# Kernel optimization log

Hardware: AMD Instinct MI355X
Metric: run time of the kernel (lower is better)

Reference implementation:

```python
import jax, jax.numpy as jnp
import numpy as np

P, A = 100000, 50000          # num papers, num authors
IN, H, OUT = 128, 256, 349    # in_channels, hidden_channels, out_channels
E_W, E_C = 600000, 1000000    # writes edges, cites edges


def setup_inputs() -> dict:
    key = jax.random.key(0)
    ks = jax.random.split(key, 24)
    s = 0.05  # weight init scale
    inp = {
        "x_paper": jax.random.normal(ks[0], (P, IN), jnp.float32),
        "emb_author": jax.random.normal(ks[1], (A, H), jnp.float32) * s,
        "lin_paper_w": jax.random.normal(ks[2], (IN, H), jnp.float32) * s,
        "lin_paper_b": jnp.zeros((H,), jnp.float32),
        "c0_root_paper_w": jax.random.normal(ks[3], (H, H), jnp.float32) * s,
        "c0_root_paper_b": jnp.zeros((H,), jnp.float32),
        "c0_root_author_w": jax.random.normal(ks[4], (H, H), jnp.float32) * s,
        "c0_root_author_b": jnp.zeros((H,), jnp.float32),
        "c0_rel_writes_w": jax.random.normal(ks[5], (H, H), jnp.float32) * s,
        "c0_rel_cites_w": jax.random.normal(ks[6], (H, H), jnp.float32) * s,
        "c0_rel_revw_w": jax.random.normal(ks[7], (H, H), jnp.float32) * s,
        "c1_root_w": jax.random.normal(ks[8], (H, OUT), jnp.float32) * s,
        "c1_root_b": jnp.zeros((OUT,), jnp.float32),
        "c1_rel_writes_w": jax.random.normal(ks[9], (H, OUT), jnp.float32) * s,
        "c1_rel_cites_w": jax.random.normal(ks[10], (H, OUT), jnp.float32) * s,
        "writes_src": jax.random.randint(ks[11], (E_W,), 0, A, jnp.int32),
        "writes_dst": jax.random.randint(ks[12], (E_W,), 0, P, jnp.int32),
        "cites_src": jax.random.randint(ks[13], (E_C,), 0, P, jnp.int32),
        "cites_dst": jax.random.randint(ks[14], (E_C,), 0, P, jnp.int32),
        "revw_src": jax.random.randint(ks[15], (E_W,), 0, P, jnp.int32),
        "revw_dst": jax.random.randint(ks[16], (E_W,), 0, A, jnp.int32),
    }
    return inp


def mean_agg(x_src, src, dst, num_dst):
    """adj_t.matmul(x, reduce='mean'): mean of source features over in-edges per dst node (0 for isolated nodes)."""
    msg = jnp.take(x_src, src, axis=0)                                  # [E, D]
    summed = jax.ops.segment_sum(msg, dst, num_segments=num_dst)        # [num_dst, D]
    cnt = jax.ops.segment_sum(jnp.ones((dst.shape[0],), x_src.dtype), dst, num_segments=num_dst)
    return summed / jnp.maximum(cnt, 1.0)[:, None]


def reference(x_paper, emb_author, lin_paper_w, lin_paper_b,
              c0_root_paper_w, c0_root_paper_b, c0_root_author_w, c0_root_author_b,
              c0_rel_writes_w, c0_rel_cites_w, c0_rel_revw_w,
              c1_root_w, c1_root_b, c1_rel_writes_w, c1_rel_cites_w,
              writes_src, writes_dst, cites_src, cites_dst, revw_src, revw_dst):
    # input projection for featured type; embedding for author
    h_p = x_paper @ lin_paper_w + lin_paper_b   # [P, H]
    h_a = emb_author                            # [A, H]

    # layer 0: root transforms + per-relation mean-agg + rel linear, accumulated by dst type
    out_p = h_p @ c0_root_paper_w + c0_root_paper_b
    out_a = h_a @ c0_root_author_w + c0_root_author_b
    out_p = out_p + mean_agg(h_a, writes_src, writes_dst, P) @ c0_rel_writes_w
    out_p = out_p + mean_agg(h_p, cites_src, cites_dst, P) @ c0_rel_cites_w
    out_a = out_a + mean_agg(h_p, revw_src, revw_dst, A) @ c0_rel_revw_w
    h_p = jax.nn.relu(out_p)
    h_a = jax.nn.relu(out_a)
    # dropout is a no-op in eval mode

    # final layer: only out_type='paper' and edge types ending at paper
    out = h_p @ c1_root_w + c1_root_b
    out = out + mean_agg(h_a, writes_src, writes_dst, P) @ c1_rel_writes_w
    out = out + mean_agg(h_p, cites_src, cites_dst, P) @ c1_rel_cites_w
    return jax.nn.log_softmax(out, axis=-1)
```

## Files before the change

kernel.cpp:

```cpp
#include <hip/hip_runtime.h>
#include <cstdint>
#include <cstddef>

#define P_NODES 100000
#define A_NODES 50000
#define IN_CH   128
#define H_CH    256
#define OUT_CH  349
#define NE_W    600000
#define NE_C    1000000

#define SCAN_BS 512

typedef unsigned short u16;
typedef unsigned int   u32;
typedef __bf16 bf16x8 __attribute__((ext_vector_type(8)));
typedef float  f32x4  __attribute__((ext_vector_type(4)));
typedef u16    u16x4  __attribute__((ext_vector_type(4)));
typedef u16    u16x8  __attribute__((ext_vector_type(8)));

__device__ __forceinline__ u16 f2bf(float f) {
    u32 u = __builtin_bit_cast(u32, f);
    u += 0x7FFFu + ((u >> 16) & 1u);
    return (u16)(u >> 16);
}
__device__ __forceinline__ float bf2f(u16 v) {
    return __builtin_bit_cast(float, (u32)v << 16);
}

typedef const __attribute__((address_space(1))) u32 gas_u32;
typedef __attribute__((address_space(3))) u32 las_u32;
__device__ __forceinline__ void gl_lds16(const void* g, void* l)
{
    __builtin_amdgcn_global_load_lds(
        reinterpret_cast<gas_u32*>(reinterpret_cast<uintptr_t>(g)),
        reinterpret_cast<las_u32*>(reinterpret_cast<uintptr_t>(l)),
        16, 0, 0);
}

template<bool OUTBF, bool RELU>
__global__ __launch_bounds__(256) void mfma_gemm(
    const u16* __restrict__ A, int lda,
    const u16* __restrict__ WT, int ldw,
    const float* __restrict__ bias, void* __restrict__ Cv, int ldc,
    int M, int N, int K)
{
    __shared__ u16 Asl[128 * 32];
    __shared__ u16 Bsl[128 * 32];

    const int tid = threadIdx.x;
    const int blockM = blockIdx.y * 128;
    const int blockN = blockIdx.x * 128;
    const int w    = tid >> 6;
    const int lane = tid & 63;
    const int m16  = lane & 15;
    const int quad = lane >> 4;
    const int wr   = (w >> 1) * 64;
    const int wc   = (w & 1) * 64;

    if (blockM + 128 > M || blockN + 128 > N) {
        for (int i = tid; i < 128 * 32; i += 256) { Asl[i] = 0; Bsl[i] = 0; }
    }
    __syncthreads();

    const int ra  = lane >> 2;
    const int rA0 = w * 32 + ra;
    const int rA1 = rA0 + 16;
    const int cs  = ((lane & 3) ^ ((rA0 >> 1) & 3)) * 8;

    const u16* gA0 = A  + (size_t)(blockM + rA0) * lda + cs;
    const u16* gA1 = A  + (size_t)(blockM + rA1) * lda + cs;
    const u16* gB0 = WT + (size_t)(blockN + rA0) * ldw + cs;
    const u16* gB1 = WT + (size_t)(blockN + rA1) * ldw + cs;
    u16* lA0 = &Asl[(w * 32) * 32];
    u16* lA1 = &Asl[(w * 32 + 16) * 32];
    u16* lB0 = &Bsl[(w * 32) * 32];
    u16* lB1 = &Bsl[(w * 32 + 16) * 32];
    const bool vA0 = blockM + rA0 < M, vA1 = blockM + rA1 < M;
    const bool vB0 = blockN + rA0 < N, vB1 = blockN + rA1 < N;

    const int swz = (quad ^ ((m16 >> 1) & 3)) * 8;

    f32x4 acc[4][4];
#pragma unroll
    for (int i = 0; i < 4; ++i)
#pragma unroll
        for (int j = 0; j < 4; ++j) acc[i][j] = (f32x4){0.f, 0.f, 0.f, 0.f};

    for (int k0 = 0; k0 < K; k0 += 32) {
        if (vA0) gl_lds16(gA0 + k0, lA0);
        if (vA1) gl_lds16(gA1 + k0, lA1);
        if (vB0) gl_lds16(gB0 + k0, lB0);
        if (vB1) gl_lds16(gB1 + k0, lB1);
        __syncthreads();

        bf16x8 af[4], bfr[4];
#pragma unroll
        for (int mt = 0; mt < 4; ++mt)
            af[mt] = *(const bf16x8*)&Asl[(wr + mt * 16 + m16) * 32 + swz];
#pragma unroll
        for (int nt = 0; nt < 4; ++nt)
            bfr[nt] = *(const bf16x8*)&Bsl[(wc + nt * 16 + m16) * 32 + swz];
#pragma unroll
        for (int mt = 0; mt < 4; ++mt)
#pragma unroll
            for (int nt = 0; nt < 4; ++nt)
                acc[mt][nt] = __builtin_amdgcn_mfma_f32_16x16x32_bf16(
                    af[mt], bfr[nt], acc[mt][nt], 0, 0, 0);
        __syncthreads();
    }

#pragma unroll
    for (int mt = 0; mt < 4; ++mt) {
#pragma unroll
        for (int nt = 0; nt < 4; ++nt) {
            int col = blockN + wc + nt * 16 + m16;
            if (col >= N) continue;
#pragma unroll
            for (int reg = 0; reg < 4; ++reg) {
                int row = blockM + wr + mt * 16 + quad * 4 + reg;
                if (row >= M) continue;
                float v = acc[mt][nt][reg];
                if (bias) v += bias[col];
                if constexpr (RELU) v = fmaxf(v, 0.f);
                size_t off = (size_t)row * ldc + col;
                if constexpr (OUTBF) ((u16*)Cv)[off] = f2bf(v);
                else                 ((float*)Cv)[off] = v;
            }
        }
    }
}

__global__ void prep_convert(const float* __restrict__ x, u16* __restrict__ x_bf,
                             const float* __restrict__ emb, u16* __restrict__ emb_bf)
{
    int i = blockIdx.x * blockDim.x + threadIdx.x;
    const int NX = P_NODES * IN_CH / 4;
    const int NE = A_NODES * H_CH / 4;
    if (i < NX) {
        float4 v = *(const float4*)(x + (size_t)i * 4);
        u16x4 o = {f2bf(v.x), f2bf(v.y), f2bf(v.z), f2bf(v.w)};
        *(u16x4*)(x_bf + (size_t)i * 4) = o;
    } else if (i < NX + NE) {
        int j = i - NX;
        int r = j >> 6, c = (j & 63) * 4;
        float4 v = *(const float4*)(emb + (size_t)r * H_CH + c);
        u16x4 o = {f2bf(v.x), f2bf(v.y), f2bf(v.z), f2bf(v.w)};
        *(u16x4*)(emb_bf + (size_t)r * 512 + c) = o;
    }
}

__global__ void transpose_all(
    const float* __restrict__ lin, const float* __restrict__ r0p,
    const float* __restrict__ c0wr, const float* __restrict__ c0ci,
    const float* __restrict__ r0a, const float* __restrict__ c0rv,
    const float* __restrict__ r1, const float* __restrict__ c1wr,
    const float* __restrict__ c1ci,
    u16* __restrict__ wt_lin, u16* __restrict__ wt_l0p,
    u16* __restrict__ wt_l0a, u16* __restrict__ wt_l1)
{
    int i = blockIdx.x * blockDim.x + threadIdx.x;
    const float* W; u16* WT; int N, ldk, koff;
    if (i < 32768)       { W = lin;  WT = wt_lin; N = 256; ldk = 128; koff = 0;   }
    else if (i < 98304)  { i -= 32768;  W = r0p;  WT = wt_l0p; N = 256; ldk = 768; koff = 0;   }
    else if (i < 163840) { i -= 98304;  W = c0wr; WT = wt_l0p; N = 256; ldk = 768; koff = 256; }
    else if (i < 229376) { i -= 163840; W = c0ci; WT = wt_l0p; N = 256; ldk = 768; koff = 512; }
    else if (i < 294912) { i -= 229376; W = r0a;  WT = wt_l0a; N = 256; ldk = 512; koff = 0;   }
    else if (i < 360448) { i -= 294912; W = c0rv; WT = wt_l0a; N = 256; ldk = 512; koff = 256; }
    else if (i < 449792) { i -= 360448; W = r1;   WT = wt_l1;  N = 349; ldk = 768; koff = 0;   }
    else if (i < 539136) { i -= 449792; W = c1wr; WT = wt_l1;  N = 349; ldk = 768; koff = 256; }
    else if (i < 628480) { i -= 539136; W = c1ci; WT = wt_l1;  N = 349; ldk = 768; koff = 512; }
    else return;
    int k = i / N, n = i - k * N;
    WT[(size_t)n * ldk + koff + k] = f2bf(W[(size_t)k * N + n]);
}

__global__ void deg3_kernel(const int* __restrict__ wd, const int* __restrict__ cd,
                            const int* __restrict__ rd,
                            int* __restrict__ deg_w, int* __restrict__ deg_c,
                            int* __restrict__ deg_r)
{
    int e = blockIdx.x * blockDim.x + threadIdx.x;
    if (e < NE_W) atomicAdd(&deg_w[wd[e]], 1);
    if (e < NE_C) atomicAdd(&deg_c[cd[e]], 1);
    if (e < NE_W) atomicAdd(&deg_r[rd[e]], 1);
}

__global__ __launch_bounds__(SCAN_BS) void scan_a3(
    const int* __restrict__ dw, const int* __restrict__ dc, const int* __restrict__ dr,
    int* __restrict__ pw, int* __restrict__ pc, int* __restrict__ pr, int* __restrict__ blk)
{
    __shared__ int s[SCAN_BS];
    int g = blockIdx.y;
    const int* deg = (g == 0) ? dw : (g == 1) ? dc : dr;
    int* ptr = (g == 0) ? pw : (g == 1) ? pc : pr;
    int n = (g == 2) ? A_NODES : P_NODES;
    int tid = threadIdx.x;
    int i = blockIdx.x * SCAN_BS + tid;
    int v = (i < n) ? deg[i] : 0;
    s[tid] = v;
    __syncthreads();
    for (int off = 1; off < SCAN_BS; off <<= 1) {
        int t = 0;
        if (tid >= off) t = s[tid - off];
        __syncthreads();
        s[tid] += t;
        __syncthreads();
    }
    if (i < n) ptr[i] = s[tid] - v;
    if (tid == SCAN_BS - 1) blk[g * 256 + blockIdx.x] = s[tid];
}

__global__ __launch_bounds__(SCAN_BS) void scan_b3(int* __restrict__ blk)
{
    __shared__ int s[SCAN_BS];
    int g = blockIdx.x;
    int tid = threadIdx.x;
    int v = (tid < 256) ? blk[g * 256 + tid] : 0;
    s[tid] = v;
    __syncthreads();
    for (int off = 1; off < SCAN_BS; off <<= 1) {
        int t = 0;
        if (tid >= off) t = s[tid - off];
        __syncthreads();
        s[tid] += t;
        __syncthreads();
    }
    if (tid < 256) blk[g * 256 + tid] = s[tid] - v;
}

__global__ void scan_c3(const int* __restrict__ dw, const int* __restrict__ dc,
                        const int* __restrict__ dr,
                        int* __restrict__ pw, int* __restrict__ pc, int* __restrict__ pr,
                        const int* __restrict__ blk,
                        int* __restrict__ cw, int* __restrict__ cc, int* __restrict__ cr,
                        float* __restrict__ iw, float* __restrict__ ic, float* __restrict__ ir)
{
    int g = blockIdx.y;
    const int* deg = (g == 0) ? dw : (g == 1) ? dc : dr;
    int* ptr = (g == 0) ? pw : (g == 1) ? pc : pr;
    int* cur = (g == 0) ? cw : (g == 1) ? cc : cr;
    float* inv = (g == 0) ? iw : (g == 1) ? ic : ir;
    int n = (g == 2) ? A_NODES : P_NODES;
    int E = (g == 1) ? NE_C : NE_W;
    int i = blockIdx.x * blockDim.x + threadIdx.x;
    if (i < n) {
        int p = ptr[i] + blk[g * 256 + i / SCAN_BS];
        ptr[i] = p;
        cur[i] = p;
        inv[i] = 1.0f / fmaxf((float)deg[i], 1.0f);
    }
    if (i == 0) ptr[n] = E;
}

__global__ __launch_bounds__(256) void fill3_kernel(
    const int* __restrict__ wsrc, const int* __restrict__ wdst,
    const int* __restrict__ csrc, const int* __restrict__ cdst,
    const int* __restrict__ rsrc, const int* __restrict__ rdst,
    int* __restrict__ cw, int* __restrict__ cc, int* __restrict__ cr,
    int* __restrict__ iw, int* __restrict__ ic, int* __restrict__ ir)
{
    const int g   = blockIdx.x & 7;
    const int bi  = blockIdx.x >> 3;
    const int nbt = (gridDim.x >> 3) * blockDim.x;
    const int t0  = bi * blockDim.x + threadIdx.x;

    const int plo = g * (P_NODES / 8), phi = plo + P_NODES / 8;
    const int alo = g * (A_NODES / 8), ahi = alo + A_NODES / 8;

    for (int e = t0; e < NE_W; e += nbt) {
        int d = wdst[e];
        if (d >= plo && d < phi) { int p = atomicAdd(&cw[d], 1); iw[p] = wsrc[e]; }
    }
    for (int e = t0; e < NE_C; e += nbt) {
        int d = cdst[e];
        if (d >= plo && d < phi) { int p = atomicAdd(&cc[d], 1); ic[p] = csrc[e]; }
    }
    for (int e = t0; e < NE_W; e += nbt) {
        int d = rdst[e];
        if (d >= alo && d < ahi) { int p = atomicAdd(&cr[d], 1); ir[p] = rsrc[e]; }
    }
}

__global__ __launch_bounds__(256) void gather_bf16(
    const u16* __restrict__ T, int ldt,
    const int* __restrict__ ptr, const int* __restrict__ idx,
    const float* __restrict__ inv, u16* __restrict__ out, int ldo, int R)
{
    int row = blockIdx.x * 8 + (threadIdx.x >> 5);
    if (row >= R) return;
    int l = (threadIdx.x & 31) * 8;
    int s = ptr[row], e = ptr[row + 1];
    float acc[8];
#pragma unroll
    for (int q = 0; q < 8; ++q) acc[q] = 0.f;
    int j = s;
    for (; j + 3 < e; j += 4) {
        int i0 = idx[j], i1 = idx[j + 1], i2 = idx[j + 2], i3 = idx[j + 3];
        u16x8 t0 = *(const u16x8*)(T + (size_t)i0 * ldt + l);
        u16x8 t1 = *(const u16x8*)(T + (size_t)i1 * ldt + l);
        u16x8 t2 = *(const u16x8*)(T + (size_t)i2 * ldt + l);
        u16x8 t3 = *(const u16x8*)(T + (size_t)i3 * ldt + l);
#pragma unroll
        for (int q = 0; q < 8; ++q)
            acc[q] += (bf2f(t0[q]) + bf2f(t1[q])) + (bf2f(t2[q]) + bf2f(t3[q]));
    }
    for (; j < e; ++j) {
        int i0 = idx[j];
        u16x8 t0 = *(const u16x8*)(T + (size_t)i0 * ldt + l);
#pragma unroll
        for (int q = 0; q < 8; ++q) acc[q] += bf2f(t0[q]);
    }
    float wgt = inv[row];
    u16x8 o;
#pragma unroll
    for (int q = 0; q < 8; ++q) o[q] = f2bf(acc[q] * wgt);
    *(u16x8*)(out + (size_t)row * ldo + l) = o;
}

__global__ __launch_bounds__(64) void log_softmax_kernel(float* __restrict__ x)
{
    const int row = blockIdx.x;
    const int lane = threadIdx.x;
    float* xr = x + (size_t)row * OUT_CH;

    float v[6];
    float m = -3.402823466e38f;
#pragma unroll
    for (int o = 0; o < 6; ++o) {
        int j = lane + o * 64;
        v[o] = (j < OUT_CH) ? xr[j] : -3.402823466e38f;
        m = fmaxf(m, v[o]);
    }
#pragma unroll
    for (int off = 32; off > 0; off >>= 1) m = fmaxf(m, __shfl_xor(m, off));

    float s = 0.f;
#pragma unroll
    for (int o = 0; o < 6; ++o) {
        int j = lane + o * 64;
        if (j < OUT_CH) s += __expf(v[o] - m);
    }
#pragma unroll
    for (int off = 32; off > 0; off >>= 1) s += __shfl_xor(s, off);

    float lse = m + __logf(s);
#pragma unroll
    for (int o = 0; o < 6; ++o) {
        int j = lane + o * 64;
        if (j < OUT_CH) xr[j] = v[o] - lse;
    }
}

extern "C" void kernel_launch(void* const* d_in, const int* in_sizes, int n_in,
                              void* d_out, int out_size, void* d_ws, size_t ws_size,
                              hipStream_t stream)
{
    const float* x_paper = (const float*)d_in[0];
    const float* emb_a   = (const float*)d_in[1];
    const float* lin_w   = (const float*)d_in[2];
    const float* lin_b   = (const float*)d_in[3];
    const float* r0p_w   = (const float*)d_in[4];
    const float* r0p_b   = (const float*)d_in[5];
    const float* r0a_w   = (const float*)d_in[6];
    const float* r0a_b   = (const float*)d_in[7];
    const float* c0_wr   = (const float*)d_in[8];
    const float* c0_ci   = (const float*)d_in[9];
    const float* c0_rv   = (const float*)d_in[10];
    const float* r1_w    = (const float*)d_in[11];
    const float* r1_b    = (const float*)d_in[12];
    const float* c1_wr   = (const float*)d_in[13];
    const float* c1_ci   = (const float*)d_in[14];
    const int*   w_src   = (const int*)d_in[15];
    const int*   w_dst   = (const int*)d_in[16];
    const int*   c_src   = (const int*)d_in[17];
    const int*   c_dst   = (const int*)d_in[18];
    const int*   r_src   = (const int*)d_in[19];
    const int*   r_dst   = (const int*)d_in[20];

    const size_t P768 = (size_t)P_NODES * 768;

    u16* big_A0 = (u16*)d_ws;
    u16* big_A1 = big_A0 + P768;
    u16* x_bf   = big_A1 + P768;
    u16* wt_lin = x_bf + (size_t)P_NODES * IN_CH;
    u16* wt_l0p = wt_lin + 32768;
    u16* wt_l0a = wt_l0p + 196608;
    u16* wt_l1  = wt_l0a + 131072;
    float* inv_w = (float*)(wt_l1 + 268032 + 64);
    float* inv_c = inv_w + P_NODES;
    float* inv_r = inv_c + P_NODES;

    int* ip    = (int*)(inv_r + A_NODES);
    int* deg_w = ip;                 ip += P_NODES;
    int* deg_c = ip;                 ip += P_NODES;
    int* deg_r = ip;                 ip += A_NODES;
    int* ptr_w = ip;                 ip += P_NODES + 1;
    int* ptr_c = ip;                 ip += P_NODES + 1;
    int* ptr_r = ip;                 ip += A_NODES + 1;
    int* cur_w = ip;                 ip += P_NODES;
    int* cur_c = ip;                 ip += P_NODES;
    int* cur_r = ip;                 ip += A_NODES;
    int* idx_w = ip;                 ip += NE_W;
    int* idx_c = ip;                 ip += NE_C;
    int* idx_r = ip;                 ip += NE_W;
    int* blk   = ip;                 ip += 3 * 256;

    u16* big_A0a  = (u16*)d_out;
    u16* out_a_bf = big_A0a + (size_t)A_NODES * 512;
    float* logits = (float*)d_out;

    {
        int n = P_NODES * IN_CH / 4 + A_NODES * H_CH / 4;
        prep_convert<<<(n + 255) / 256, 256, 0, stream>>>(x_paper, x_bf, emb_a, big_A0a);
    }
    transpose_all<<<(628480 + 255) / 256, 256, 0, stream>>>(
        lin_w, r0p_w, c0_wr, c0_ci, r0a_w, c0_rv, r1_w, c1_wr, c1_ci,
        wt_lin, wt_l0p, wt_l0a, wt_l1);

    hipMemsetAsync(deg_w, 0, (size_t)(2 * P_NODES + A_NODES) * sizeof(int), stream);
    deg3_kernel<<<(NE_C + 255) / 256, 256, 0, stream>>>(w_dst, c_dst, r_dst, deg_w, deg_c, deg_r);
    {
        dim3 ga((P_NODES + SCAN_BS - 1) / SCAN_BS, 3);
        scan_a3<<<ga, SCAN_BS, 0, stream>>>(deg_w, deg_c, deg_r, ptr_w, ptr_c, ptr_r, blk);
        scan_b3<<<3, SCAN_BS, 0, stream>>>(blk);
        dim3 gc((P_NODES + 255) / 256, 3);
        scan_c3<<<gc, 256, 0, stream>>>(deg_w, deg_c, deg_r, ptr_w, ptr_c, ptr_r, blk,
                                        cur_w, cur_c, cur_r, inv_w, inv_c, inv_r);
    }
    fill3_kernel<<<2048, 256, 0, stream>>>(
        w_src, w_dst, c_src, c_dst, r_src, r_dst, cur_w, cur_c, cur_r, idx_w, idx_c, idx_r);

    auto gat = [&](const u16* T, int ldt, const int* ptr, const int* idx,
                   const float* inv, u16* out, int ldo, int R) {
        gather_bf16<<<(R + 7) / 8, 256, 0, stream>>>(T, ldt, ptr, idx, inv, out, ldo, R);
    };

    {
        dim3 grid(2, (P_NODES + 127) / 128);
        mfma_gemm<true, false><<<grid, 256, 0, stream>>>(
            x_bf, IN_CH, wt_lin, 128, lin_b, big_A0, 768, P_NODES, H_CH, IN_CH);
    }
    gat(big_A0a, 512, ptr_w, idx_w, inv_w, big_A0 + 256, 768, P_NODES);
    gat(big_A0, 768, ptr_c, idx_c, inv_c, big_A0 + 512, 768, P_NODES);
    gat(big_A0, 768, ptr_r, idx_r, inv_r, big_A0a + 256, 512, A_NODES);

    {
        dim3 grid(2, (P_NODES + 127) / 128);
        mfma_gemm<true, true><<<grid, 256, 0, stream>>>(
            big_A0, 768, wt_l0p, 768, r0p_b, big_A1, 768, P_NODES, H_CH, 768);
    }
    {
        dim3 grid(2, (A_NODES + 127) / 128);
        mfma_gemm<true, true><<<grid, 256, 0, stream>>>(
            big_A0a, 512, wt_l0a, 512, r0a_b, out_a_bf, 256, A_NODES, H_CH, 512);
    }
    gat(out_a_bf, 256, ptr_w, idx_w, inv_w, big_A1 + 256, 768, P_NODES);
    gat(big_A1, 768, ptr_c, idx_c, inv_c, big_A1 + 512, 768, P_NODES);

    {
        dim3 grid(3, (P_NODES + 127) / 128);
        mfma_gemm<false, false><<<grid, 256, 0, stream>>>(
            big_A1, 768, wt_l1, 768, r1_b, logits, OUT_CH, P_NODES, OUT_CH, 768);
    }

    log_softmax_kernel<<<P_NODES, 64, 0, stream>>>(logits);
}
```

Before: 1.111 ms.

## Widen GEMM tiles to multiple N-blocks per workgroup with grouped block ordering

The MFMA GEMM is templated on NT so each workgroup computes a 128xNT*128 output tile, reusing each loaded A tile across NT B tiles. Blocks are remapped through a 1D grid grouped in 8 M-tiles for L2 locality. All GEMMs use NT=2, so the 256-wide layers are covered by one workgroup per M tile. The cost is twice the accumulators per thread, which raises register pressure and may lower occupancy, and the final 349-column GEMM wastes more work in its padded tile.

```diff
diff --git a/kernel.cpp b/kernel.cpp
--- a/kernel.cpp
+++ b/kernel.cpp
@@ -38,7 +38,7 @@
         16, 0, 0);
 }
 
-template<bool OUTBF, bool RELU>
+template<int NT, bool OUTBF, bool RELU>
 __global__ __launch_bounds__(256) void mfma_gemm(
     const u16* __restrict__ A, int lda,
     const u16* __restrict__ WT, int ldw,
@@ -46,11 +46,22 @@
     int M, int N, int K)
 {
     __shared__ u16 Asl[128 * 32];
-    __shared__ u16 Bsl[128 * 32];
+    __shared__ u16 Bsl[NT * 128 * 32];
+
+    const int mt_blocks = (M + 127) >> 7;
+    const int ntb = (N + NT * 128 - 1) / (NT * 128);
+    {
+    }
+    const int bid  = blockIdx.x;
+    const int grp  = bid / (8 * ntb);
+    const int rr   = bid - grp * (8 * ntb);
+    const int mtile = grp * 8 + (rr & 7);
+    const int nidx  = rr >> 3;
+    if (mtile >= mt_blocks) return;
+    const int blockM  = mtile * 128;
+    const int blockN0 = nidx * (NT * 128);
 
     const int tid = threadIdx.x;
-    const int blockM = blockIdx.y * 128;
-    const int blockN = blockIdx.x * 128;
     const int w    = tid >> 6;
     const int lane = tid & 63;
     const int m16  = lane & 15;
@@ -58,8 +69,9 @@
     const int wr   = (w >> 1) * 64;
     const int wc   = (w & 1) * 64;
 
-    if (blockM + 128 > M || blockN + 128 > N) {
-        for (int i = tid; i < 128 * 32; i += 256) { Asl[i] = 0; Bsl[i] = 0; }
+    if (blockM + 128 > M || blockN0 + NT * 128 > N) {
+        for (int i = tid; i < 128 * 32; i += 256) Asl[i] = 0;
+        for (int i = tid; i < NT * 128 * 32; i += 256) Bsl[i] = 0;
     }
     __syncthreads();
 
@@ -68,67 +80,94 @@
     const int rA1 = rA0 + 16;
     const int cs  = ((lane & 3) ^ ((rA0 >> 1) & 3)) * 8;
 
-    const u16* gA0 = A  + (size_t)(blockM + rA0) * lda + cs;
-    const u16* gA1 = A  + (size_t)(blockM + rA1) * lda + cs;
-    const u16* gB0 = WT + (size_t)(blockN + rA0) * ldw + cs;
-    const u16* gB1 = WT + (size_t)(blockN + rA1) * ldw + cs;
+    const u16* gA0 = A + (size_t)(blockM + rA0) * lda + cs;
+    const u16* gA1 = A + (size_t)(blockM + rA1) * lda + cs;
     u16* lA0 = &Asl[(w * 32) * 32];
     u16* lA1 = &Asl[(w * 32 + 16) * 32];
-    u16* lB0 = &Bsl[(w * 32) * 32];
-    u16* lB1 = &Bsl[(w * 32 + 16) * 32];
     const bool vA0 = blockM + rA0 < M, vA1 = blockM + rA1 < M;
-    const bool vB0 = blockN + rA0 < N, vB1 = blockN + rA1 < N;
+
+    const u16* gB0[NT]; const u16* gB1[NT];
+    u16* lB0[NT]; u16* lB1[NT];
+    bool vB0[NT], vB1[NT];
+#pragma unroll
+    for (int j = 0; j < NT; ++j) {
+        gB0[j] = WT + (size_t)(blockN0 + j * 128 + rA0) * ldw + cs;
+        gB1[j] = WT + (size_t)(blockN0 + j * 128 + rA1) * ldw + cs;
+        lB0[j] = &Bsl[j * 4096 + (w * 32) * 32];
+        lB1[j] = &Bsl[j * 4096 + (w * 32 + 16) * 32];
+        vB0[j] = blockN0 + j * 128 + rA0 < N;
+        vB1[j] = blockN0 + j * 128 + rA1 < N;
+    }
 
     const int swz = (quad ^ ((m16 >> 1) & 3)) * 8;
 
-    f32x4 acc[4][4];
-#pragma unroll
-    for (int i = 0; i < 4; ++i)
-#pragma unroll
-        for (int j = 0; j < 4; ++j) acc[i][j] = (f32x4){0.f, 0.f, 0.f, 0.f};
+    f32x4 acc[NT][4][4];
+#pragma unroll
+    for (int j = 0; j < NT; ++j)
+#pragma unroll
+        for (int i = 0; i < 4; ++i)
+#pragma unroll
+            for (int n = 0; n < 4; ++n) acc[j][i][n] = (f32x4){0.f, 0.f, 0.f, 0.f};
 
     for (int k0 = 0; k0 < K; k0 += 32) {
         if (vA0) gl_lds16(gA0 + k0, lA0);
         if (vA1) gl_lds16(gA1 + k0, lA1);
-        if (vB0) gl_lds16(gB0 + k0, lB0);
-        if (vB1) gl_lds16(gB1 + k0, lB1);
-        __syncthreads();
-
-        bf16x8 af[4], bfr[4];
+#pragma unroll
+        for (int j = 0; j < NT; ++j) {
+            if (vB0[j]) gl_lds16(gB0[j] + k0, lB0[j]);
+            if (vB1[j]) gl_lds16(gB1[j] + k0, lB1[j]);
+        }
+        __syncthreads();
+
+        bf16x8 af[4], bfr[NT][4];
 #pragma unroll
         for (int mt = 0; mt < 4; ++mt)
             af[mt] = *(const bf16x8*)&Asl[(wr + mt * 16 + m16) * 32 + swz];
 #pragma unroll
-        for (int nt = 0; nt < 4; ++nt)
-            bfr[nt] = *(const bf16x8*)&Bsl[(wc + nt * 16 + m16) * 32 + swz];
-#pragma unroll
-        for (int mt = 0; mt < 4; ++mt)
+        for (int j = 0; j < NT; ++j)
 #pragma unroll
             for (int nt = 0; nt < 4; ++nt)
-                acc[mt][nt] = __builtin_amdgcn_mfma_f32_16x16x32_bf16(
-                    af[mt], bfr[nt], acc[mt][nt], 0, 0, 0);
-        __syncthreads();
-    }
-
-#pragma unroll
-    for (int mt = 0; mt < 4; ++mt) {
-#pragma unroll
-        for (int nt = 0; nt < 4; ++nt) {
-            int col = blockN + wc + nt * 16 + m16;
-            if (col >= N) continue;
-#pragma unroll
-            for (int reg = 0; reg < 4; ++reg) {
-                int row = blockM + wr + mt * 16 + quad * 4 + reg;
-                if (row >= M) continue;
-                float v = acc[mt][nt][reg];
-                if (bias) v += bias[col];
-                if constexpr (RELU) v = fmaxf(v, 0.f);
-                size_t off = (size_t)row * ldc + col;
-                if constexpr (OUTBF) ((u16*)Cv)[off] = f2bf(v);
-                else                 ((float*)Cv)[off] = v;
+                bfr[j][nt] = *(const bf16x8*)&Bsl[j * 4096 + (wc + nt * 16 + m16) * 32 + swz];
+#pragma unroll
+        for (int j = 0; j < NT; ++j)
+#pragma unroll
+            for (int mt = 0; mt < 4; ++mt)
+#pragma unroll
+                for (int nt = 0; nt < 4; ++nt)
+                    acc[j][mt][nt] = __builtin_amdgcn_mfma_f32_16x16x32_bf16(
+                        af[mt], bfr[j][nt], acc[j][mt][nt], 0, 0, 0);
+        __syncthreads();
+    }
+
+#pragma unroll
+    for (int j = 0; j < NT; ++j) {
+#pragma unroll
+        for (int mt = 0; mt < 4; ++mt) {
+#pragma unroll
+            for (int nt = 0; nt < 4; ++nt) {
+                int col = blockN0 + j * 128 + wc + nt * 16 + m16;
+                if (col >= N) continue;
+#pragma unroll
+                for (int reg = 0; reg < 4; ++reg) {
+                    int row = blockM + wr + mt * 16 + quad * 4 + reg;
+                    if (row >= M) continue;
+                    float v = acc[j][mt][nt][reg];
+                    if (bias) v += bias[col];
+                    if constexpr (RELU) v = fmaxf(v, 0.f);
+                    size_t off = (size_t)row * ldc + col;
+                    if constexpr (OUTBF) ((u16*)Cv)[off] = f2bf(v);
+                    else                 ((float*)Cv)[off] = v;
+                }
             }
         }
     }
+}
+
+static inline int gemm_grid(int M, int N, int NT)
+{
+    int mt = (M + 127) / 128;
+    int ntb = (N + NT * 128 - 1) / (NT * 128);
+    return ((mt + 7) / 8) * 8 * ntb;
 }
 
 __global__ void prep_convert(const float* __restrict__ x, u16* __restrict__ x_bf,
@@ -436,33 +475,24 @@
         gather_bf16<<<(R + 7) / 8, 256, 0, stream>>>(T, ldt, ptr, idx, inv, out, ldo, R);
     };
 
-    {
-        dim3 grid(2, (P_NODES + 127) / 128);
-        mfma_gemm<true, false><<<grid, 256, 0, stream>>>(
-            x_bf, IN_CH, wt_lin, 128, lin_b, big_A0, 768, P_NODES, H_CH, IN_CH);
-    }
+    mfma_gemm<2, true, false><<<gemm_grid(P_NODES, 256, 2), 256, 0, stream>>>(
+        x_bf, IN_CH, wt_lin, 128, lin_b, big_A0, 768, P_NODES, H_CH, IN_CH);
+
     gat(big_A0a, 512, ptr_w, idx_w, inv_w, big_A0 + 256, 768, P_NODES);
     gat(big_A0, 768, ptr_c, idx_c, inv_c, big_A0 + 512, 768, P_NODES);
     gat(big_A0, 768, ptr_r, idx_r, inv_r, big_A0a + 256, 512, A_NODES);
 
-    {
-        dim3 grid(2, (P_NODES + 127) / 128);
-        mfma_gemm<true, true><<<grid, 256, 0, stream>>>(
-            big_A0, 768, wt_l0p, 768, r0p_b, big_A1, 768, P_NODES, H_CH, 768);
-    }
-    {
-        dim3 grid(2, (A_NODES + 127) / 128);
-        mfma_gemm<true, true><<<grid, 256, 0, stream>>>(
-            big_A0a, 512, wt_l0a, 512, r0a_b, out_a_bf, 256, A_NODES, H_CH, 512);
-    }
+    mfma_gemm<2, true, true><<<gemm_grid(P_NODES, 256, 2), 256, 0, stream>>>(
+        big_A0, 768, wt_l0p, 768, r0p_b, big_A1, 768, P_NODES, H_CH, 768);
+
+    mfma_gemm<2, true, true><<<gemm_grid(A_NODES, 256, 2), 256, 0, stream>>>(
+        big_A0a, 512, wt_l0a, 512, r0a_b, out_a_bf, 256, A_NODES, H_CH, 512);
+
     gat(out_a_bf, 256, ptr_w, idx_w, inv_w, big_A1 + 256, 768, P_NODES);
     gat(big_A1, 768, ptr_c, idx_c, inv_c, big_A1 + 512, 768, P_NODES);
 
-    {
-        dim3 grid(3, (P_NODES + 127) / 128);
-        mfma_gemm<false, false><<<grid, 256, 0, stream>>>(
-            big_A1, 768, wt_l1, 768, r1_b, logits, OUT_CH, P_NODES, OUT_CH, 768);
-    }
+    mfma_gemm<2, false, false><<<gemm_grid(P_NODES, OUT_CH, 2), 256, 0, stream>>>(
+        big_A1, 768, wt_l1, 768, r1_b, logits, OUT_CH, P_NODES, OUT_CH, 768);
 
     log_softmax_kernel<<<P_NODES, 64, 0, stream>>>(logits);
 }
```

New measurement: 1.420 ms. 27.9% more time.
